# Kernel tuning notes

Hardware: AMD Instinct MI355X
Metric: run time of the kernel (lower is better)

## Reference

```python
import jax, jax.numpy as jnp
import numpy as np

T, B, S = 32, 32, 64
I = H = C = 1024  # input_size == hidden_size required by the original module's wiring
A = 128           # attention_size


def setup_inputs() -> dict:
    key = jax.random.key(0)
    ks = jax.random.split(key, 10)
    s_ih = 1.0 / np.sqrt(H)
    s_a = 1.0 / np.sqrt(H + C)
    return {
        "inputs": jax.random.normal(ks[0], (T, B, I), jnp.float32),
        "context": jax.random.normal(ks[1], (S, B, C), jnp.float32),
        # LSTMCell params (PyTorch layout: gates ordered i, f, g, o)
        "W_ih": jax.random.normal(ks[2], (4 * H, I), jnp.float32) * s_ih,
        "W_hh": jax.random.normal(ks[3], (4 * H, H), jnp.float32) * s_ih,
        "b_ih": jax.random.normal(ks[4], (4 * H,), jnp.float32) * s_ih,
        "b_hh": jax.random.normal(ks[5], (4 * H,), jnp.float32) * s_ih,
        # Attention params: linear1 [A, H+C], linear2 [1, A]
        "W1": jax.random.normal(ks[6], (A, H + C), jnp.float32) * s_a,
        "b1": jax.random.normal(ks[7], (A,), jnp.float32) * s_a,
        "W2": jax.random.normal(ks[8], (1, A), jnp.float32) * (1.0 / np.sqrt(A)),
        "b2": jax.random.normal(ks[9], (1,), jnp.float32) * (1.0 / np.sqrt(A)),
    }


def reference(inputs, context, W_ih, W_hh, b_ih, b_hh, W1, b1, W2, b2):
    Tn, Bn, _ = inputs.shape
    Hn = W_hh.shape[1]
    xt = jnp.transpose(context, (1, 0, 2))  # [B, S, C]
    # Split linear1 weight into hidden-part and context-part so the
    # context projection can be hoisted out of the time loop (same math
    # as concatenating [y, xt] then applying linear1).
    W1_y = W1[:, :Hn]          # [A, H]
    W1_x = W1[:, Hn:]          # [A, C]
    ctx_proj = jnp.einsum('bsc,ac->bsa', xt, W1_x)  # [B, S, A]
    bias = b_ih + b_hh

    def step(carry, x_t):
        h, c = carry
        gates = x_t @ W_ih.T + h @ W_hh.T + bias   # [B, 4H]
        i, f, g, o = jnp.split(gates, 4, axis=-1)
        c_new = jax.nn.sigmoid(f) * c + jax.nn.sigmoid(i) * jnp.tanh(g)
        h_new = jax.nn.sigmoid(o) * jnp.tanh(c_new)
        # additive attention: linear1 (no nonlinearity in original) -> linear2 -> softmax
        hid = h_new[:, None, :] @ W1_y.T[None] + ctx_proj + b1  # [B, S, A]
        scores = jnp.einsum('bsa,a->bs', hid, W2[0]) + b2[0]    # [B, S]
        attn = jax.nn.softmax(scores, axis=-1)
        weighted = jnp.einsum('bs,bsc->bc', attn, xt)           # [B, C]
        return (h_new, c_new), (weighted, attn)

    h0 = jnp.zeros((Bn, Hn), inputs.dtype)
    (h, c), (outputs, attentions) = jax.lax.scan(step, (h0, h0), inputs)
    return outputs, h, c, attentions
```

## Files before the change

kernel.cpp:

```cpp
#include <hip/hip_runtime.h>

#define T_ 32
#define B_ 32
#define S_ 64
#define C_ 1024
#define H_ 1024
#define NWG 64
#define HSLOT 32768

typedef __attribute__((ext_vector_type(8))) short bf16x8;
typedef __attribute__((ext_vector_type(4))) float f32x4;

#define OUT_H   1048576
#define OUT_CC  1081344
#define OUT_AT  1114112

__device__ __forceinline__ ushort f2b(float f) {
  unsigned u = __float_as_uint(f);
  unsigned r = (u + 0x7FFFu + ((u >> 16) & 1u)) >> 16;
  return (ushort)r;
}
__device__ __forceinline__ float b2f(ushort h) {
  return __uint_as_float(((unsigned)h) << 16);
}

__global__ __launch_bounds__(256) void k_cvt3(const float* __restrict__ s0, ushort* __restrict__ d0,
                                              const float* __restrict__ s1, ushort* __restrict__ d1,
                                              const float* __restrict__ s2, ushort* __restrict__ d2) {
  int blk = blockIdx.x;
  const float* src;
  ushort* dst;
  int base;
  if (blk < 512) { src = s0; dst = d0; base = blk; }
  else if (blk < 2560) { src = s1; dst = d1; base = blk - 512; }
  else { src = s2; dst = d2; base = blk - 2560; }
  size_t i = ((size_t)base * 256 + threadIdx.x) * 8;
  float4 v0 = *reinterpret_cast<const float4*>(src + i);
  float4 v1 = *reinterpret_cast<const float4*>(src + i + 4);
  uint4 o;
  o.x = (unsigned)f2b(v0.x) | ((unsigned)f2b(v0.y) << 16);
  o.y = (unsigned)f2b(v0.z) | ((unsigned)f2b(v0.w) << 16);
  o.z = (unsigned)f2b(v1.x) | ((unsigned)f2b(v1.y) << 16);
  o.w = (unsigned)f2b(v1.z) | ((unsigned)f2b(v1.w) << 16);
  *reinterpret_cast<uint4*>(dst + i) = o;
}

__global__ __launch_bounds__(256) void k_prep(const float* __restrict__ W1, const float* __restrict__ W2,
                                              const float* __restrict__ bih, const float* __restrict__ bhh,
                                              float* __restrict__ v, float* __restrict__ bias,
                                              ushort* __restrict__ hring, unsigned* __restrict__ flags) {
  int blk = blockIdx.x, tid = threadIdx.x;
  if (blk < 4) {
    int c = blk * 256 + tid;
    float acc = 0.f;
#pragma unroll 8
    for (int a = 0; a < 128; ++a) acc += W1[a * 2048 + 1024 + c] * W2[a];
    v[c] = acc;
  } else if (blk < 20) {
    int j = (blk - 4) * 256 + tid;
    bias[j] = bih[j] + bhh[j];
  } else if (blk < 24) {
    unsigned* hz = reinterpret_cast<unsigned*>(hring);
    int base = (blk - 20) * 4096;
    for (int i = 0; i < 16; ++i) hz[base + i * 256 + tid] = 0u;
  } else {
    for (int i = 0; i < 4; ++i) flags[i * 256 + tid] = 0u;
  }
}

__global__ __launch_bounds__(256) void k_attn(const float* __restrict__ ctx, const float* __restrict__ v,
                                              float* __restrict__ out) {
  int b = blockIdx.x, tid = threadIdx.x;
  int lane = tid & 63, w = tid >> 6;
  __shared__ float v_s[1024];
  __shared__ float sc_s[64];
  __shared__ float att_s[64];
  for (int i = 0; i < 4; ++i) v_s[tid + i * 256] = v[tid + i * 256];
  __syncthreads();
  for (int si = 0; si < 16; ++si) {
    int s = w * 16 + si;
    const float* xr = ctx + (size_t)(s * B_ + b) * C_;
    float acc = 0.f;
#pragma unroll
    for (int i = 0; i < 16; ++i) { int c = lane + i * 64; acc += xr[c] * v_s[c]; }
    for (int off = 32; off; off >>= 1) acc += __shfl_down(acc, off);
    if (lane == 0) sc_s[s] = acc;
  }
  __syncthreads();
  if (tid < 64) {
    float val = sc_s[tid];
    float mx = val;
    for (int off = 32; off; off >>= 1) mx = fmaxf(mx, __shfl_xor(mx, off));
    float e = expf(val - mx);
    float sm = e;
    for (int off = 32; off; off >>= 1) sm += __shfl_xor(sm, off);
    att_s[tid] = e / sm;
  }
  __syncthreads();
  const float4* ctx4 = reinterpret_cast<const float4*>(ctx);
  float4 a4 = {0.f, 0.f, 0.f, 0.f};
  for (int s = 0; s < 64; ++s) {
    float a = att_s[s];
    float4 x = ctx4[(size_t)(s * B_ + b) * 256 + tid];
    a4.x += a * x.x; a4.y += a * x.y; a4.z += a * x.z; a4.w += a * x.w;
  }
#pragma unroll 4
  for (int t = 0; t < T_; ++t)
    reinterpret_cast<float4*>(out + (size_t)(t * B_ + b) * C_)[tid] = a4;
  if (tid < 64) {
    float av = att_s[tid];
#pragma unroll 4
    for (int t = 0; t < T_; ++t) out[OUT_AT + (t * B_ + b) * 64 + tid] = av;
  }
}

__global__ __launch_bounds__(256) void k_xproj(const ushort* __restrict__ inpb, const ushort* __restrict__ Wihb,
                                               const float* __restrict__ bias, ushort* __restrict__ xpT) {
  __shared__ int4 A_s[512];
  __shared__ int4 B_s[512];
  int tid = threadIdx.x;
  int m0 = (blockIdx.x >> 5) << 7;
  int j0 = (blockIdx.x & 31) << 7;
  int lane = tid & 63, w = tid >> 6;
  int wm = (w >> 1) * 64, wn = (w & 1) * 64;
  int g = lane >> 4, r = lane & 15;
  f32x4 acc[4][4];
#pragma unroll
  for (int mi = 0; mi < 4; ++mi)
#pragma unroll
    for (int ni = 0; ni < 4; ++ni) acc[mi][ni] = (f32x4)(0.f);

  int f0 = tid, r0s = f0 >> 2, g0s = f0 & 3;
  int f1 = tid + 256, r1s = f1 >> 2, g1s = f1 & 3;
  for (int k0 = 0; k0 < 1024; k0 += 32) {
    __syncthreads();
    A_s[g0s * 128 + r0s] = *reinterpret_cast<const int4*>(inpb + (size_t)(m0 + r0s) * 1024 + k0 + g0s * 8);
    B_s[g0s * 128 + r0s] = *reinterpret_cast<const int4*>(Wihb + (size_t)(j0 + r0s) * 1024 + k0 + g0s * 8);
    A_s[g1s * 128 + r1s] = *reinterpret_cast<const int4*>(inpb + (size_t)(m0 + r1s) * 1024 + k0 + g1s * 8);
    B_s[g1s * 128 + r1s] = *reinterpret_cast<const int4*>(Wihb + (size_t)(j0 + r1s) * 1024 + k0 + g1s * 8);
    __syncthreads();
    bf16x8 af[4], bf_[4];
#pragma unroll
    for (int mi = 0; mi < 4; ++mi) af[mi] = *reinterpret_cast<const bf16x8*>(&A_s[g * 128 + wm + mi * 16 + r]);
#pragma unroll
    for (int ni = 0; ni < 4; ++ni) bf_[ni] = *reinterpret_cast<const bf16x8*>(&B_s[g * 128 + wn + ni * 16 + r]);
#pragma unroll
    for (int mi = 0; mi < 4; ++mi)
#pragma unroll
      for (int ni = 0; ni < 4; ++ni)
        acc[mi][ni] = __builtin_amdgcn_mfma_f32_16x16x32_bf16(af[mi], bf_[ni], acc[mi][ni], 0, 0, 0);
  }
  int q = lane >> 4;
#pragma unroll
  for (int ni = 0; ni < 4; ++ni) {
    int j = j0 + wn + ni * 16 + r;
    float bj = bias[j];
#pragma unroll
    for (int mi = 0; mi < 4; ++mi) {
      int mb = m0 + wm + mi * 16 + q * 4;
      uint2 pk;
      pk.x = (unsigned)f2b(acc[mi][ni][0] + bj) | ((unsigned)f2b(acc[mi][ni][1] + bj) << 16);
      pk.y = (unsigned)f2b(acc[mi][ni][2] + bj) | ((unsigned)f2b(acc[mi][ni][3] + bj) << 16);
      *reinterpret_cast<uint2*>(xpT + (size_t)j * 1024 + mb) = pk;
    }
  }
}

__global__ __launch_bounds__(1024, 4) void k_rec(const ushort* __restrict__ Whhb, const ushort* __restrict__ xpT,
                                                 ushort* __restrict__ hring,
                                                 float* __restrict__ out, unsigned* __restrict__ flags) {
  int tid = threadIdx.x, lane = tid & 63, w = tid >> 6;
  int wg = blockIdx.x;
  int q = w & 3, ks = w >> 2;
  int g = lane >> 4, r = lane & 15;
  int hidx0 = wg * 16 + q * 4;
  int kbase = ks * 256;
  int j = (r >> 2) * 1024 + hidx0 + (r & 3);
  bf16x8 a[8];
  {
    const ushort* ap = Whhb + (size_t)j * 1024 + kbase + g * 8;
#pragma unroll
    for (int kk = 0; kk < 8; ++kk) a[kk] = *reinterpret_cast<const bf16x8*>(ap + kk * 32);
  }
  __shared__ uint4 hl4[4096];
  __shared__ float red[4][4][16][32];
  __shared__ __align__(16) ushort hs[32][16];
  float c_reg = 0.f;
  int eb = tid & 31, hl = (tid >> 5) & 3, qq = tid >> 7;
  int ehidx = wg * 16 + qq * 4 + hl;

  float xf_i = 0.f, xf_f = 0.f, xf_g = 0.f, xf_o = 0.f;
  if (tid < 512) {
    xf_i = b2f(xpT[(size_t)(ehidx) * 1024 + eb]);
    xf_f = b2f(xpT[(size_t)(1024 + ehidx) * 1024 + eb]);
    xf_g = b2f(xpT[(size_t)(2048 + ehidx) * 1024 + eb]);
    xf_o = b2f(xpT[(size_t)(3072 + ehidx) * 1024 + eb]);
  }

#pragma unroll 1
  for (int t = 0; t < T_; ++t) {
    const uint4* hin4 = reinterpret_cast<const uint4*>(hring + (size_t)t * HSLOT);
    ushort* hout = hring + (size_t)(t + 1) * HSLOT;
    {
      uint4 v0 = hin4[tid];
      uint4 v1 = hin4[tid + 1024];
      uint4 v2 = hin4[tid + 2048];
      uint4 v3 = hin4[tid + 3072];
      int ch0 = tid, ch1 = tid + 1024, ch2 = tid + 2048, ch3 = tid + 3072;
      hl4[(ch0 >> 7) * 128 + ((ch0 & 127) ^ ((ch0 >> 7) & 7))] = v0;
      hl4[(ch1 >> 7) * 128 + ((ch1 & 127) ^ ((ch1 >> 7) & 7))] = v1;
      hl4[(ch2 >> 7) * 128 + ((ch2 & 127) ^ ((ch2 >> 7) & 7))] = v2;
      hl4[(ch3 >> 7) * 128 + ((ch3 & 127) ^ ((ch3 >> 7) & 7))] = v3;
    }
    __syncthreads();
    f32x4 acc0 = (f32x4)(0.f), acc1 = (f32x4)(0.f);
    int cb = ks * 32 + g;
#pragma unroll
    for (int kk = 0; kk < 8; ++kk) {
      int c16 = cb + kk * 4;
      bf16x8 b0 = *reinterpret_cast<const bf16x8*>(&hl4[r * 128 + (c16 ^ (r & 7))]);
      bf16x8 b1 = *reinterpret_cast<const bf16x8*>(&hl4[(r + 16) * 128 + (c16 ^ (r & 7))]);
      acc0 = __builtin_amdgcn_mfma_f32_16x16x32_bf16(a[kk], b0, acc0, 0, 0, 0);
      acc1 = __builtin_amdgcn_mfma_f32_16x16x32_bf16(a[kk], b1, acc1, 0, 0, 0);
    }
#pragma unroll
    for (int e = 0; e < 4; ++e) {
      red[q][ks][g * 4 + e][r] = acc0[e];
      red[q][ks][g * 4 + e][r + 16] = acc1[e];
    }
    __syncthreads();
    if (tid < 512) {
      float ig = red[qq][0][0 + hl][eb]  + red[qq][1][0 + hl][eb]  + red[qq][2][0 + hl][eb]  + red[qq][3][0 + hl][eb]  + xf_i;
      float fg = red[qq][0][4 + hl][eb]  + red[qq][1][4 + hl][eb]  + red[qq][2][4 + hl][eb]  + red[qq][3][4 + hl][eb]  + xf_f;
      float gg = red[qq][0][8 + hl][eb]  + red[qq][1][8 + hl][eb]  + red[qq][2][8 + hl][eb]  + red[qq][3][8 + hl][eb]  + xf_g;
      float og = red[qq][0][12 + hl][eb] + red[qq][1][12 + hl][eb] + red[qq][2][12 + hl][eb] + red[qq][3][12 + hl][eb] + xf_o;
      float si = 1.f / (1.f + __expf(-ig));
      float sf = 1.f / (1.f + __expf(-fg));
      float so = 1.f / (1.f + __expf(-og));
      float c_new = sf * c_reg + si * tanhf(gg);
      float h_new = so * tanhf(c_new);
      c_reg = c_new;
      hs[eb][qq * 4 + hl] = f2b(h_new);
      if (t == T_ - 1) {
        out[OUT_H + eb * 1024 + ehidx] = h_new;
        out[OUT_CC + eb * 1024 + ehidx] = c_new;
      }
    }
    if (t != T_ - 1) {
      __syncthreads();
      int mnext = (t + 1) * 32 + eb;
      if (w == 0) {
        int b = lane >> 1, half = lane & 1;
        uint4 vv = *reinterpret_cast<const uint4*>(&hs[b][half * 8]);
        unsigned* hp = reinterpret_cast<unsigned*>(hout) + b * 512 + wg * 8 + half * 4;
        __hip_atomic_store(hp + 0, vv.x, __ATOMIC_RELAXED, __HIP_MEMORY_SCOPE_AGENT);
        __hip_atomic_store(hp + 1, vv.y, __ATOMIC_RELAXED, __HIP_MEMORY_SCOPE_AGENT);
        __hip_atomic_store(hp + 2, vv.z, __ATOMIC_RELAXED, __HIP_MEMORY_SCOPE_AGENT);
        __hip_atomic_store(hp + 3, vv.w, __ATOMIC_RELAXED, __HIP_MEMORY_SCOPE_AGENT);
        asm volatile("s_waitcnt vmcnt(0)" ::: "memory");
        if (lane == 0)
          __hip_atomic_store(&flags[wg * 16], (unsigned)(t + 1), __ATOMIC_RELAXED, __HIP_MEMORY_SCOPE_AGENT);
      }
      float nx_i = 0.f, nx_f = 0.f, nx_g = 0.f, nx_o = 0.f;
      if (tid < 512) {
        nx_i = b2f(xpT[(size_t)(ehidx) * 1024 + mnext]);
        nx_f = b2f(xpT[(size_t)(1024 + ehidx) * 1024 + mnext]);
        nx_g = b2f(xpT[(size_t)(2048 + ehidx) * 1024 + mnext]);
        nx_o = b2f(xpT[(size_t)(3072 + ehidx) * 1024 + mnext]);
      }
      if (w == 0) {
        unsigned tgt = (unsigned)(t + 1);
        for (;;) {
          unsigned vfl = __hip_atomic_load(&flags[lane * 16], __ATOMIC_RELAXED, __HIP_MEMORY_SCOPE_AGENT);
          if (__all(vfl >= tgt)) break;
          __builtin_amdgcn_s_sleep(1);
        }
      }
      __syncthreads();
      xf_i = nx_i; xf_f = nx_f; xf_g = nx_g; xf_o = nx_o;
    }
  }
}

extern "C" void kernel_launch(void* const* d_in, const int* in_sizes, int n_in,
                              void* d_out, int out_size, void* d_ws, size_t ws_size,
                              hipStream_t stream) {
  const float* inp = (const float*)d_in[0];
  const float* ctx = (const float*)d_in[1];
  const float* Wih = (const float*)d_in[2];
  const float* Whh = (const float*)d_in[3];
  const float* bih = (const float*)d_in[4];
  const float* bhh = (const float*)d_in[5];
  const float* W1  = (const float*)d_in[6];
  const float* W2  = (const float*)d_in[8];
  float* out = (float*)d_out;
  char* wsb = (char*)d_ws;

  float* v    = (float*)(wsb + 0);
  float* bias = (float*)(wsb + 4096);
  ushort* hring = (ushort*)(wsb + 32768);
  ushort* inpb = (ushort*)(wsb + 2195456);
  ushort* Wihb = (ushort*)(wsb + 4292608);
  ushort* Whhb = (ushort*)(wsb + 12681216);
  ushort* xpT  = (ushort*)(wsb + 21069824);
  unsigned* flags = (unsigned*)(wsb + 29458432);

  hipLaunchKernelGGL(k_prep, dim3(25), dim3(256), 0, stream, W1, W2, bih, bhh, v, bias, hring, flags);
  hipLaunchKernelGGL(k_cvt3, dim3(4608), dim3(256), 0, stream, inp, inpb, Wih, Wihb, Whh, Whhb);
  hipLaunchKernelGGL(k_attn, dim3(32), dim3(256), 0, stream, ctx, v, out);
  hipLaunchKernelGGL(k_xproj, dim3(256), dim3(256), 0, stream, inpb, Wihb, bias, xpT);

  const ushort* Whhb_c = Whhb;
  const ushort* xpT_c = xpT;
  void* kargs[5];
  kargs[0] = (void*)&Whhb_c;
  kargs[1] = (void*)&xpT_c;
  kargs[2] = (void*)&hring;
  kargs[3] = (void*)&out;
  kargs[4] = (void*)&flags;
  hipLaunchCooperativeKernel((const void*)k_rec, dim3(NWG), dim3(1024), kargs, 0, stream);
}
```

Before: 223.2 us.

## Fuse prep kernels, convert W_hh in-kernel, per-wave flag waits, overlap output broadcast

Merges the prep and conversion kernels into one launch. W_hh is now converted from fp32 to bf16 directly into registers inside the recurrent kernel, which drops a separate conversion pass. The recurrent step no longer stages h into LDS behind a block barrier: each wave polls only the producer flags it needs and reads h straight from global memory. The per-timestep broadcast of the attention-weighted output moves from k_attn into the recurrent loop, where it can overlap the serial recurrence. The cost is uncached global h reads per wave, plus a weaker memory-ordering guarantee because the flag loads are relaxed.

```diff
diff --git a/kernel.cpp b/kernel.cpp
--- a/kernel.cpp
+++ b/kernel.cpp
@@ -24,44 +24,38 @@
   return __uint_as_float(((unsigned)h) << 16);
 }
 
-__global__ __launch_bounds__(256) void k_cvt3(const float* __restrict__ s0, ushort* __restrict__ d0,
-                                              const float* __restrict__ s1, ushort* __restrict__ d1,
-                                              const float* __restrict__ s2, ushort* __restrict__ d2) {
-  int blk = blockIdx.x;
-  const float* src;
-  ushort* dst;
-  int base;
-  if (blk < 512) { src = s0; dst = d0; base = blk; }
-  else if (blk < 2560) { src = s1; dst = d1; base = blk - 512; }
-  else { src = s2; dst = d2; base = blk - 2560; }
-  size_t i = ((size_t)base * 256 + threadIdx.x) * 8;
-  float4 v0 = *reinterpret_cast<const float4*>(src + i);
-  float4 v1 = *reinterpret_cast<const float4*>(src + i + 4);
-  uint4 o;
-  o.x = (unsigned)f2b(v0.x) | ((unsigned)f2b(v0.y) << 16);
-  o.y = (unsigned)f2b(v0.z) | ((unsigned)f2b(v0.w) << 16);
-  o.z = (unsigned)f2b(v1.x) | ((unsigned)f2b(v1.y) << 16);
-  o.w = (unsigned)f2b(v1.z) | ((unsigned)f2b(v1.w) << 16);
-  *reinterpret_cast<uint4*>(dst + i) = o;
-}
-
-__global__ __launch_bounds__(256) void k_prep(const float* __restrict__ W1, const float* __restrict__ W2,
+__global__ __launch_bounds__(256) void k_init(const float* __restrict__ inp, ushort* __restrict__ inpb,
+                                              const float* __restrict__ Wih, ushort* __restrict__ Wihb,
+                                              const float* __restrict__ W1, const float* __restrict__ W2,
                                               const float* __restrict__ bih, const float* __restrict__ bhh,
                                               float* __restrict__ v, float* __restrict__ bias,
                                               ushort* __restrict__ hring, unsigned* __restrict__ flags) {
   int blk = blockIdx.x, tid = threadIdx.x;
-  if (blk < 4) {
-    int c = blk * 256 + tid;
+  if (blk < 2560) {
+    const float* src; ushort* dst; int base;
+    if (blk < 512) { src = inp; dst = inpb; base = blk; }
+    else { src = Wih; dst = Wihb; base = blk - 512; }
+    size_t i = ((size_t)base * 256 + tid) * 8;
+    float4 v0 = *reinterpret_cast<const float4*>(src + i);
+    float4 v1 = *reinterpret_cast<const float4*>(src + i + 4);
+    uint4 o;
+    o.x = (unsigned)f2b(v0.x) | ((unsigned)f2b(v0.y) << 16);
+    o.y = (unsigned)f2b(v0.z) | ((unsigned)f2b(v0.w) << 16);
+    o.z = (unsigned)f2b(v1.x) | ((unsigned)f2b(v1.y) << 16);
+    o.w = (unsigned)f2b(v1.z) | ((unsigned)f2b(v1.w) << 16);
+    *reinterpret_cast<uint4*>(dst + i) = o;
+  } else if (blk < 2564) {
+    int c = (blk - 2560) * 256 + tid;
     float acc = 0.f;
 #pragma unroll 8
     for (int a = 0; a < 128; ++a) acc += W1[a * 2048 + 1024 + c] * W2[a];
     v[c] = acc;
-  } else if (blk < 20) {
-    int j = (blk - 4) * 256 + tid;
+  } else if (blk < 2580) {
+    int j = (blk - 2564) * 256 + tid;
     bias[j] = bih[j] + bhh[j];
-  } else if (blk < 24) {
+  } else if (blk < 2584) {
     unsigned* hz = reinterpret_cast<unsigned*>(hring);
-    int base = (blk - 20) * 4096;
+    int base = (blk - 2580) * 4096;
     for (int i = 0; i < 16; ++i) hz[base + i * 256 + tid] = 0u;
   } else {
     for (int i = 0; i < 4; ++i) flags[i * 256 + tid] = 0u;
@@ -69,7 +63,7 @@
 }
 
 __global__ __launch_bounds__(256) void k_attn(const float* __restrict__ ctx, const float* __restrict__ v,
-                                              float* __restrict__ out) {
+                                              float* __restrict__ wgt, float* __restrict__ out) {
   int b = blockIdx.x, tid = threadIdx.x;
   int lane = tid & 63, w = tid >> 6;
   __shared__ float v_s[1024];
@@ -104,9 +98,7 @@
     float4 x = ctx4[(size_t)(s * B_ + b) * 256 + tid];
     a4.x += a * x.x; a4.y += a * x.y; a4.z += a * x.z; a4.w += a * x.w;
   }
-#pragma unroll 4
-  for (int t = 0; t < T_; ++t)
-    reinterpret_cast<float4*>(out + (size_t)(t * B_ + b) * C_)[tid] = a4;
+  reinterpret_cast<float4*>(wgt + b * 1024)[tid] = a4;
   if (tid < 64) {
     float av = att_s[tid];
 #pragma unroll 4
@@ -166,8 +158,8 @@
   }
 }
 
-__global__ __launch_bounds__(1024, 4) void k_rec(const ushort* __restrict__ Whhb, const ushort* __restrict__ xpT,
-                                                 ushort* __restrict__ hring,
+__global__ __launch_bounds__(1024, 4) void k_rec(const float* __restrict__ Whh, const ushort* __restrict__ xpT,
+                                                 ushort* __restrict__ hring, const float* __restrict__ wgt,
                                                  float* __restrict__ out, unsigned* __restrict__ flags) {
   int tid = threadIdx.x, lane = tid & 63, w = tid >> 6;
   int wg = blockIdx.x;
@@ -178,16 +170,25 @@
   int j = (r >> 2) * 1024 + hidx0 + (r & 3);
   bf16x8 a[8];
   {
-    const ushort* ap = Whhb + (size_t)j * 1024 + kbase + g * 8;
-#pragma unroll
-    for (int kk = 0; kk < 8; ++kk) a[kk] = *reinterpret_cast<const bf16x8*>(ap + kk * 32);
-  }
-  __shared__ uint4 hl4[4096];
+    const float* ap = Whh + (size_t)j * 1024 + kbase + g * 8;
+#pragma unroll
+    for (int kk = 0; kk < 8; ++kk) {
+      float4 f0 = *reinterpret_cast<const float4*>(ap + kk * 32);
+      float4 f1 = *reinterpret_cast<const float4*>(ap + kk * 32 + 4);
+      bf16x8 t8;
+      t8[0] = (short)f2b(f0.x); t8[1] = (short)f2b(f0.y);
+      t8[2] = (short)f2b(f0.z); t8[3] = (short)f2b(f0.w);
+      t8[4] = (short)f2b(f1.x); t8[5] = (short)f2b(f1.y);
+      t8[6] = (short)f2b(f1.z); t8[7] = (short)f2b(f1.w);
+      a[kk] = t8;
+    }
+  }
   __shared__ float red[4][4][16][32];
   __shared__ __align__(16) ushort hs[32][16];
   float c_reg = 0.f;
   int eb = tid & 31, hl = (tid >> 5) & 3, qq = tid >> 7;
   int ehidx = wg * 16 + qq * 4 + hl;
+  int pidx = (ks * 16 + (lane & 15)) * 16;
 
   float xf_i = 0.f, xf_f = 0.f, xf_g = 0.f, xf_o = 0.f;
   if (tid < 512) {
@@ -199,27 +200,19 @@
 
 #pragma unroll 1
   for (int t = 0; t < T_; ++t) {
-    const uint4* hin4 = reinterpret_cast<const uint4*>(hring + (size_t)t * HSLOT);
-    ushort* hout = hring + (size_t)(t + 1) * HSLOT;
-    {
-      uint4 v0 = hin4[tid];
-      uint4 v1 = hin4[tid + 1024];
-      uint4 v2 = hin4[tid + 2048];
-      uint4 v3 = hin4[tid + 3072];
-      int ch0 = tid, ch1 = tid + 1024, ch2 = tid + 2048, ch3 = tid + 3072;
-      hl4[(ch0 >> 7) * 128 + ((ch0 & 127) ^ ((ch0 >> 7) & 7))] = v0;
-      hl4[(ch1 >> 7) * 128 + ((ch1 & 127) ^ ((ch1 >> 7) & 7))] = v1;
-      hl4[(ch2 >> 7) * 128 + ((ch2 & 127) ^ ((ch2 >> 7) & 7))] = v2;
-      hl4[(ch3 >> 7) * 128 + ((ch3 & 127) ^ ((ch3 >> 7) & 7))] = v3;
-    }
-    __syncthreads();
+    if (t > 0) {
+      for (;;) {
+        unsigned vfl = __hip_atomic_load(&flags[pidx], __ATOMIC_RELAXED, __HIP_MEMORY_SCOPE_AGENT);
+        if (__all((int)(vfl >= (unsigned)t))) break;
+        __builtin_amdgcn_s_sleep(1);
+      }
+    }
+    const ushort* bp = hring + (size_t)t * HSLOT + (size_t)r * 1024 + kbase + g * 8;
     f32x4 acc0 = (f32x4)(0.f), acc1 = (f32x4)(0.f);
-    int cb = ks * 32 + g;
 #pragma unroll
     for (int kk = 0; kk < 8; ++kk) {
-      int c16 = cb + kk * 4;
-      bf16x8 b0 = *reinterpret_cast<const bf16x8*>(&hl4[r * 128 + (c16 ^ (r & 7))]);
-      bf16x8 b1 = *reinterpret_cast<const bf16x8*>(&hl4[(r + 16) * 128 + (c16 ^ (r & 7))]);
+      bf16x8 b0 = *reinterpret_cast<const bf16x8*>(bp + kk * 32);
+      bf16x8 b1 = *reinterpret_cast<const bf16x8*>(bp + 16 * 1024 + kk * 32);
       acc0 = __builtin_amdgcn_mfma_f32_16x16x32_bf16(a[kk], b0, acc0, 0, 0, 0);
       acc1 = __builtin_amdgcn_mfma_f32_16x16x32_bf16(a[kk], b1, acc1, 0, 0, 0);
     }
@@ -246,10 +239,10 @@
         out[OUT_CC + eb * 1024 + ehidx] = c_new;
       }
     }
+    __syncthreads();
     if (t != T_ - 1) {
-      __syncthreads();
-      int mnext = (t + 1) * 32 + eb;
       if (w == 0) {
+        ushort* hout = hring + (size_t)(t + 1) * HSLOT;
         int b = lane >> 1, half = lane & 1;
         uint4 vv = *reinterpret_cast<const uint4*>(&hs[b][half * 8]);
         unsigned* hp = reinterpret_cast<unsigned*>(hout) + b * 512 + wg * 8 + half * 4;
@@ -263,21 +256,18 @@
       }
       float nx_i = 0.f, nx_f = 0.f, nx_g = 0.f, nx_o = 0.f;
       if (tid < 512) {
+        int mnext = (t + 1) * 32 + eb;
         nx_i = b2f(xpT[(size_t)(ehidx) * 1024 + mnext]);
         nx_f = b2f(xpT[(size_t)(1024 + ehidx) * 1024 + mnext]);
         nx_g = b2f(xpT[(size_t)(2048 + ehidx) * 1024 + mnext]);
         nx_o = b2f(xpT[(size_t)(3072 + ehidx) * 1024 + mnext]);
       }
-      if (w == 0) {
-        unsigned tgt = (unsigned)(t + 1);
-        for (;;) {
-          unsigned vfl = __hip_atomic_load(&flags[lane * 16], __ATOMIC_RELAXED, __HIP_MEMORY_SCOPE_AGENT);
-          if (__all(vfl >= tgt)) break;
-          __builtin_amdgcn_s_sleep(1);
-        }
-      }
-      __syncthreads();
       xf_i = nx_i; xf_f = nx_f; xf_g = nx_g; xf_o = nx_o;
+    }
+    if (tid < 128) {
+      int off = ((wg & 1) << 9) + (tid << 2);
+      float4 vv = *reinterpret_cast<const float4*>(wgt + ((wg >> 1) << 10) + off);
+      *reinterpret_cast<float4*>(out + ((size_t)(t * 32 + (wg >> 1)) << 10) + off) = vv;
     }
   }
 }
@@ -296,27 +286,29 @@
   float* out = (float*)d_out;
   char* wsb = (char*)d_ws;
 
-  float* v    = (float*)(wsb + 0);
-  float* bias = (float*)(wsb + 4096);
-  ushort* hring = (ushort*)(wsb + 32768);
-  ushort* inpb = (ushort*)(wsb + 2195456);
-  ushort* Wihb = (ushort*)(wsb + 4292608);
-  ushort* Whhb = (ushort*)(wsb + 12681216);
-  ushort* xpT  = (ushort*)(wsb + 21069824);
-  unsigned* flags = (unsigned*)(wsb + 29458432);
-
-  hipLaunchKernelGGL(k_prep, dim3(25), dim3(256), 0, stream, W1, W2, bih, bhh, v, bias, hring, flags);
-  hipLaunchKernelGGL(k_cvt3, dim3(4608), dim3(256), 0, stream, inp, inpb, Wih, Wihb, Whh, Whhb);
-  hipLaunchKernelGGL(k_attn, dim3(32), dim3(256), 0, stream, ctx, v, out);
+  float* v     = (float*)(wsb + 0);
+  float* bias  = (float*)(wsb + 4096);
+  float* wgt   = (float*)(wsb + 20480);
+  ushort* hring = (ushort*)(wsb + 151552);
+  ushort* inpb = (ushort*)(wsb + 2314240);
+  ushort* Wihb = (ushort*)(wsb + 4411392);
+  ushort* xpT  = (ushort*)(wsb + 12800000);
+  unsigned* flags = (unsigned*)(wsb + 21188608);
+
+  hipLaunchKernelGGL(k_init, dim3(2585), dim3(256), 0, stream,
+                     inp, inpb, Wih, Wihb, W1, W2, bih, bhh, v, bias, hring, flags);
+  hipLaunchKernelGGL(k_attn, dim3(32), dim3(256), 0, stream, ctx, v, wgt, out);
   hipLaunchKernelGGL(k_xproj, dim3(256), dim3(256), 0, stream, inpb, Wihb, bias, xpT);
 
-  const ushort* Whhb_c = Whhb;
+  const float* Whh_c = Whh;
   const ushort* xpT_c = xpT;
-  void* kargs[5];
-  kargs[0] = (void*)&Whhb_c;
+  const float* wgt_c = wgt;
+  void* kargs[6];
+  kargs[0] = (void*)&Whh_c;
   kargs[1] = (void*)&xpT_c;
   kargs[2] = (void*)&hring;
-  kargs[3] = (void*)&out;
-  kargs[4] = (void*)&flags;
+  kargs[3] = (void*)&wgt_c;
+  kargs[4] = (void*)&out;
+  kargs[5] = (void*)&flags;
   hipLaunchCooperativeKernel((const void*)k_rec, dim3(NWG), dim3(1024), kargs, 0, stream);
 }
```

Measured after the change: 387.8 us. +73.8%, slower.
